# Optimization experiments

Measured on AMD Instinct MI355X. Metric: run time of the kernel, lower is better.

Reference implementation:

```python
import jax, jax.numpy as jnp
import numpy as np

N = 50000        # nodes
E = 800000       # edges (avg degree 16)
F_IN = 128       # num_features
DIM = 128        # hidden dim
C = 10           # num_classes
TEMP = 0.6       # EntropyLinear default temperature
SLOPE = 0.01     # F.leaky_relu default negative slope


def setup_inputs() -> dict:
    key = jax.random.key(0)
    ks = jax.random.split(key, 12)
    x = jax.random.normal(ks[0], (N, F_IN), dtype=jnp.float32)
    edge_index = jax.random.randint(ks[1], (2, E), 0, N, dtype=jnp.int32)
    s_in = 1.0 / np.sqrt(F_IN)
    s_d = 1.0 / np.sqrt(DIM)
    W0 = jax.random.normal(ks[2], (F_IN, DIM), jnp.float32) * s_in
    b0 = jnp.zeros((DIM,), jnp.float32)
    W1 = jax.random.normal(ks[3], (DIM, DIM), jnp.float32) * s_d
    b1 = jnp.zeros((DIM,), jnp.float32)
    W2 = jax.random.normal(ks[4], (DIM, DIM), jnp.float32) * s_d
    b2 = jnp.zeros((DIM,), jnp.float32)
    W3 = jax.random.normal(ks[5], (DIM, DIM), jnp.float32) * s_d
    b3 = jnp.zeros((DIM,), jnp.float32)
    lens_w = jax.random.normal(ks[6], (C, 1, DIM), jnp.float32) * s_d  # (n_classes, out=1, in)
    lens_b = jax.random.normal(ks[7], (C, 1, 1), jnp.float32) * 0.01
    return dict(x=x, edge_index=edge_index, W0=W0, b0=b0, W1=W1, b1=b1,
                W2=W2, b2=b2, W3=W3, b3=b3, lens_w=lens_w, lens_b=lens_b)


def _gcn_conv(h, W, b, src, dst, norm):
    # PyG GCNConv: h' = scatter_add( norm_e * (h W)[src] ) + b
    m = h @ W                                  # [N, out]
    msg = m[src] * norm[:, None]               # [E+N, out] gather + scale
    agg = jax.ops.segment_sum(msg, dst, num_segments=N)
    return agg + b


def reference(x, edge_index, W0, b0, W1, b1, W2, b2, W3, b3, lens_w, lens_b):
    loops = jnp.arange(N, dtype=edge_index.dtype)
    src = jnp.concatenate([edge_index[0], loops])   # add self-loops
    dst = jnp.concatenate([edge_index[1], loops])
    deg = jax.ops.segment_sum(jnp.ones_like(dst, jnp.float32), dst, num_segments=N)
    dis = jnp.where(deg > 0, jax.lax.rsqrt(jnp.maximum(deg, 1.0)), 0.0)
    norm = dis[src] * dis[dst]                      # symmetric D^-1/2 A D^-1/2

    h = x
    for W, b in ((W0, b0), (W1, b1), (W2, b2), (W3, b3)):
        h = _gcn_conv(h, W, b, src, dst, norm)
        h = jax.nn.leaky_relu(h, SLOPE)

    p = jax.nn.softmax(h, axis=-1)
    concepts = p / jnp.max(p, axis=-1, keepdims=True)   # [N, DIM]

    # torch_explain EntropyLinear(DIM, 1, n_classes=C)
    gamma = jnp.abs(lens_w).sum(axis=1)                 # [C, DIM] L1 over out_features
    alpha = jax.nn.softmax(gamma / TEMP, axis=1)
    alpha_norm = alpha / jnp.max(alpha, axis=1, keepdims=True)
    z = concepts[None, :, :] * alpha_norm[:, None, :]   # [C, N, DIM]
    out = jnp.einsum('cnd,cod->cno', z, lens_w) + lens_b  # [C, N, 1]
    out = jnp.transpose(out, (1, 0, 2))                 # [N, C, 1]

    log_probs = jax.nn.log_softmax(out, axis=0).squeeze(-1)  # softmax over nodes
    return concepts, log_probs
```

## Files before the change

kernel.cpp:

```cpp
#include <hip/hip_runtime.h>


#define DIMF 128
#define GRID 1024
#define TPB  256

typedef __bf16 bf16x8 __attribute__((ext_vector_type(8)));
typedef float f32x4 __attribute__((ext_vector_type(4)));

static __device__ __forceinline__ ushort f2bf(float f) {
    uint u = __float_as_uint(f);
    u += 0x7fffu + ((u >> 16) & 1u);
    return (ushort)(u >> 16);
}
static __device__ __forceinline__ float bflo(uint u) { return __uint_as_float(u << 16); }
static __device__ __forceinline__ float bfhi(uint u) { return __uint_as_float(u & 0xffff0000u); }

static __device__ __forceinline__ void upadd(float* acc, const int4& u) {
    const uint* w = (const uint*)&u;
#pragma unroll
    for (int k = 0; k < 4; ++k) {
        acc[2 * k]     += bflo(w[k]);
        acc[2 * k + 1] += bfhi(w[k]);
    }
}


union SMem {
    ushort ws[16384];
    struct { int h[256]; } ha;
    struct { int tmp[256]; } sc;
    struct { int h[256]; int lb[256]; } sa;
    struct { int cnt[256]; int cur[256]; int tmp[256]; } pb;
    struct { float wcT[1280]; float lb[16]; } ep;
    struct { float2 red[4]; } r1;
    struct { float red[2]; } wc;
    struct { float2 red2[176]; float Ls[16]; } l3;
};


static __device__ __forceinline__ void gsync(uint* cb, uint r, uint& pop, uint xcc) {
    __syncthreads();
    if (threadIdx.x == 0) {
        uint* axc   = cb + 128 + 32 * xcc;
        uint* xdone = cb + 640 + 32 * xcc;
        uint* root  = cb + 32;
        if (pop == 0) {
            while (__hip_atomic_load(cb, __ATOMIC_RELAXED, __HIP_MEMORY_SCOPE_AGENT) < (uint)GRID)
                __builtin_amdgcn_s_sleep(2);
            pop = __hip_atomic_load(cb + 64 + xcc, __ATOMIC_RELAXED, __HIP_MEMORY_SCOPE_AGENT);
        }
        uint v = __hip_atomic_fetch_add(axc, 1u, __ATOMIC_RELAXED, __HIP_MEMORY_SCOPE_AGENT) + 1;
        if (v == r * pop) {
            __hip_atomic_fetch_add(root, pop, __ATOMIC_RELEASE, __HIP_MEMORY_SCOPE_AGENT);
            while (__hip_atomic_load(root, __ATOMIC_RELAXED, __HIP_MEMORY_SCOPE_AGENT) < r * (uint)GRID)
                __builtin_amdgcn_s_sleep(2);
            asm volatile("buffer_inv\n\tbuffer_inv sc1\n\ts_waitcnt vmcnt(0)" ::: "memory");
            __hip_atomic_store(xdone, r, __ATOMIC_RELAXED, __HIP_MEMORY_SCOPE_AGENT);
        } else {
            while (__hip_atomic_load(xdone, __ATOMIC_RELAXED, __HIP_MEMORY_SCOPE_AGENT) < r)
                __builtin_amdgcn_s_sleep(2);
            asm volatile("buffer_inv\n\ts_waitcnt vmcnt(0)" ::: "memory");
        }
    }
    __syncthreads();
}


static __device__ __forceinline__ void ldws(ushort* ws, const ushort* WTsL, int tid) {
    const int4* src = (const int4*)WTsL;
    int4* dst = (int4*)ws;
#pragma unroll
    for (int i = 0; i < 8; ++i) dst[tid + 256 * i] = src[tid + 256 * i];
}

static __device__ __forceinline__ void mfma_store(const ushort* ws, const int4* a,
        const float* dis, ushort* M, int nrows, int it, int tid) {
    int wave = tid >> 6, lane = tid & 63;
    int lo = lane & 15, hi = lane >> 4;
    f32x4 acc[8];
#pragma unroll
    for (int ct = 0; ct < 8; ++ct) acc[ct] = (f32x4){0.f, 0.f, 0.f, 0.f};
#pragma unroll
    for (int kc = 0; kc < 4; ++kc) {
        bf16x8 av = __builtin_bit_cast(bf16x8, a[kc]);
#pragma unroll
        for (int ct = 0; ct < 8; ++ct) {
            int col = ct * 16 + lo;
            int byte = (col * 256 + kc * 64 + hi * 16) ^ ((col & 7) << 4);
            bf16x8 bv = *(const bf16x8*)((const char*)ws + byte);
            acc[ct] = __builtin_amdgcn_mfma_f32_16x16x32_bf16(av, bv, acc[ct], 0, 0, 0);
        }
    }
    int rbase = it * 64 + wave * 16 + hi * 4;
#pragma unroll
    for (int r = 0; r < 4; ++r) {
        int orow = rbase + r;
        if (orow < nrows) {
            float dn = dis[orow];
#pragma unroll
            for (int ct = 0; ct < 8; ++ct)
                M[((size_t)(ct >> 1) * nrows + orow) * 32 + (ct & 1) * 16 + lo]
                    = f2bf(dn * acc[ct][r]);
        }
    }
}

static __device__ __forceinline__ void gemm_phase(ushort* ws, const ushort* H,
        const ushort* WTsL, const float* dis, ushort* M, int n, int bid, int tid) {
    int nI = (n + 63) >> 6;
    for (int it = bid; it < nI; it += GRID) {
        __syncthreads();
        ldws(ws, WTsL, tid);
        int wave = tid >> 6, lane = tid & 63;
        int lo = lane & 15, hi = lane >> 4;
        int arow = it * 64 + wave * 16 + lo;
        bool inb = arow < n;
        int4 a[4];
        const int4* h4 = (const int4*)H;
#pragma unroll
        for (int kc = 0; kc < 4; ++kc) {
            int4 z = {0, 0, 0, 0};
            a[kc] = inb ? h4[((size_t)kc * n + arow) * 4 + hi] : z;
        }
        __syncthreads();
        mfma_store(ws, a, dis, M, n, it, tid);
    }
}

static __device__ __forceinline__ void gemm0_phase(ushort* ws, const float* X,
        const ushort* WTsL, const float* dis, ushort* M, int n, int bid, int tid) {
    int nI = (n + 63) >> 6;
    for (int it = bid; it < nI; it += GRID) {
        __syncthreads();
        ldws(ws, WTsL, tid);
        int wave = tid >> 6, lane = tid & 63;
        int lo = lane & 15, hi = lane >> 4;
        int arow = it * 64 + wave * 16 + lo;
        bool inb = arow < n;
        int4 a[4];
        const float4* x4 = (const float4*)X;
#pragma unroll
        for (int kc = 0; kc < 4; ++kc) {
            float4 f0 = make_float4(0.f, 0.f, 0.f, 0.f), f1 = f0;
            if (inb) {
                f0 = x4[(size_t)arow * 32 + kc * 8 + hi * 2];
                f1 = x4[(size_t)arow * 32 + kc * 8 + hi * 2 + 1];
            }
            ushort u[8] = { f2bf(f0.x), f2bf(f0.y), f2bf(f0.z), f2bf(f0.w),
                            f2bf(f1.x), f2bf(f1.y), f2bf(f1.z), f2bf(f1.w) };
            a[kc] = *(const int4*)u;
        }
        __syncthreads();
        mfma_store(ws, a, dis, M, n, it, tid);
    }
}


static __device__ __forceinline__ void agg_phase(const int4* Ms4, const ushort* csr,
        const int* offs, const float* dis, const float* bias, int4* Hs4,
        int n, int bid, int tid) {
    int nI = ((n + 63) >> 6) * 4;
    for (int it = bid; it < nI; it += GRID) {
        int slice = it & 3;
        int node = (it >> 2) * 64 + (tid >> 2);
        if (node >= n) continue;
        int q = tid & 3;
        const int4* M = Ms4 + (size_t)slice * n * 4;
        int beg = offs[node], end = offs[node + 1];

        float acc[8];
        {
            int4 u = M[(size_t)node * 4 + q];
            const uint* w = (const uint*)&u;
#pragma unroll
            for (int k = 0; k < 4; ++k) { acc[2 * k] = bflo(w[k]); acc[2 * k + 1] = bfhi(w[k]); }
        }

        int ee = beg;
        for (; ee + 4 <= end; ee += 4) {
            int s0 = csr[ee], s1 = csr[ee + 1], s2 = csr[ee + 2], s3 = csr[ee + 3];
            int4 u0 = M[(size_t)s0 * 4 + q];
            int4 u1 = M[(size_t)s1 * 4 + q];
            int4 u2 = M[(size_t)s2 * 4 + q];
            int4 u3 = M[(size_t)s3 * 4 + q];
            upadd(acc, u0); upadd(acc, u1); upadd(acc, u2); upadd(acc, u3);
        }
        for (; ee < end; ++ee) {
            int4 u0 = M[(size_t)csr[ee] * 4 + q];
            upadd(acc, u0);
        }

        float dn = dis[node];
        const float2* b2 = (const float2*)bias + slice * 16 + q * 4;
        uint o[4];
#pragma unroll
        for (int k = 0; k < 4; ++k) {
            float2 bk = b2[k];
            float v0 = dn * acc[2 * k] + bk.x, v1 = dn * acc[2 * k + 1] + bk.y;
            v0 = v0 > 0.f ? v0 : 0.01f * v0;
            v1 = v1 > 0.f ? v1 : 0.01f * v1;
            o[k] = (uint)f2bf(v0) | ((uint)f2bf(v1) << 16);
        }
        Hs4[(size_t)slice * n * 4 + (size_t)node * 4 + q] = *(const int4*)o;
    }
}


__global__ __launch_bounds__(TPB, 4) void mega_k(
        const float* __restrict__ x, const int* __restrict__ esrc,
        const int* __restrict__ edst,
        const float* __restrict__ W0f, const float* __restrict__ W1f,
        const float* __restrict__ W2f, const float* __restrict__ W3f,
        const float* __restrict__ b0, const float* __restrict__ b1,
        const float* __restrict__ b2, const float* __restrict__ b3,
        const float* __restrict__ lens_w, const float* __restrict__ lens_b,
        uint* cb, int* bcnt, int* gbase, int* gcur, int* offs, float* dis,
        uint* stage, ushort* csr, ushort* mbuf, ushort* hA, ushort* hB,
        ushort* WTs, float* outbuf, float* wcomb, float2* part,
        float* conc, float* logp, int n, int e, int ncls) {
    __shared__ SMem sm;
    const int bid = blockIdx.x;
    const int tid = threadIdx.x;
    const int NB = (n + 255) >> 8;
    const int EB = (e + 1023) >> 10;
    uint rr = 0;

    uint xcc;
    asm volatile("s_getreg_b32 %0, hwreg(HW_REG_XCC_ID)" : "=s"(xcc));
    xcc &= 15;
    uint pop = 0;
    if (tid == 0) {
        __hip_atomic_fetch_add(cb + 64 + xcc, 1u, __ATOMIC_RELAXED, __HIP_MEMORY_SCOPE_AGENT);
        asm volatile("s_waitcnt vmcnt(0)" ::: "memory");
        __hip_atomic_fetch_add(cb, 1u, __ATOMIC_RELAXED, __HIP_MEMORY_SCOPE_AGENT);
    }

    {
        int nI = EB + 256 + ncls;
        for (int it = bid; it < nI; it += GRID) {
            __syncthreads();
            if (it < EB) {
                sm.ha.h[tid] = 0;
                __syncthreads();
                int base = it * 1024;
#pragma unroll
                for (int k = 0; k < 4; ++k) {
                    int i = base + k * 256 + tid;
                    if (i < e) atomicAdd(&sm.ha.h[edst[i] >> 8], 1);
                }
                __syncthreads();
                if (sm.ha.h[tid]) atomicAdd(&bcnt[tid], sm.ha.h[tid]);
            } else if (it < EB + 256) {
                int wi = it - EB;
                const float* W = (wi >= 192) ? W3f : (wi >= 128) ? W2f
                               : (wi >= 64) ? W1f : W0f;
                ushort* outp = WTs + (size_t)(wi >> 6) * 16384;
                int idx = (wi & 63) * 256 + tid;
                int col = idx >> 7, k = idx & 127;
                float w = W[k * 128 + col];
                int byte = ((col * 128 + k) * 2) ^ ((col & 7) << 4);
                *(ushort*)((char*)outp + byte) = f2bf(w);
            } else {
                int c = it - EB - 256;
                float w = 0.f, g = 0.f, m = -1.f;
                if (tid < 128) { w = lens_w[c * 128 + tid]; g = fabsf(w); m = g; }
#pragma unroll
                for (int off = 32; off; off >>= 1) m = fmaxf(m, __shfl_xor(m, off));
                if (tid < 128 && (tid & 63) == 0) sm.wc.red[tid >> 6] = m;
                __syncthreads();
                if (tid < 128) {
                    m = fmaxf(sm.wc.red[0], sm.wc.red[1]);
                    wcomb[c * 128 + tid] = __expf((g - m) * (1.0f / 0.6f)) * w;
                }
            }
        }
    }
    gsync(cb, ++rr, pop, xcc);

    if (bid == 0) {
        int v = (tid < NB) ? bcnt[tid] : 0;
        sm.sc.tmp[tid] = v;
        __syncthreads();
        int run = v;
        for (int off = 1; off < 256; off <<= 1) {
            int a = (tid >= off) ? sm.sc.tmp[tid - off] : 0;
            __syncthreads();
            run += a;
            sm.sc.tmp[tid] = run;
            __syncthreads();
        }
        if (tid < NB) { gbase[tid] = run - v; gcur[tid] = run - v; }
        if (tid == 0) gbase[NB] = e;
    }
    gsync(cb, ++rr, pop, xcc);

    for (int it = bid; it < EB; it += GRID) {
        __syncthreads();
        sm.sa.h[tid] = 0;
        __syncthreads();
        int base = it * 1024;
        int r[4], bk[4];
        uint val[4];
#pragma unroll
        for (int k = 0; k < 4; ++k) {
            int i = base + k * 256 + tid;
            if (i < e) {
                int s = esrc[i], d = edst[i];
                bk[k] = d >> 8;
                val[k] = ((uint)(d & 255) << 16) | (uint)s;
                r[k] = atomicAdd(&sm.sa.h[bk[k]], 1);
            } else bk[k] = -1;
        }
        __syncthreads();
        if (sm.sa.h[tid]) sm.sa.lb[tid] = atomicAdd(&gcur[tid], sm.sa.h[tid]);
        __syncthreads();
#pragma unroll
        for (int k = 0; k < 4; ++k)
            if (bk[k] >= 0) stage[sm.sa.lb[bk[k]] + r[k]] = val[k];
    }
    gsync(cb, ++rr, pop, xcc);

    for (int it = bid; it < NB; it += GRID) {
        __syncthreads();
        int e0 = gbase[it], e1 = gbase[it + 1];
        sm.pb.cnt[tid] = 0;
        __syncthreads();
        for (int i = e0 + tid; i < e1; i += 256) atomicAdd(&sm.pb.cnt[stage[i] >> 16], 1);
        __syncthreads();
        int v = sm.pb.cnt[tid];
        int run = v;
        sm.pb.tmp[tid] = run;
        __syncthreads();
        for (int off = 1; off < 256; off <<= 1) {
            int a = (tid >= off) ? sm.pb.tmp[tid - off] : 0;
            __syncthreads();
            run += a;
            sm.pb.tmp[tid] = run;
            __syncthreads();
        }
        int ex = e0 + run - v;
        int node = it * 256 + tid;
        if (node < n) {
            offs[node] = ex;
            dis[node] = rsqrtf((float)(v + 1));
        }
        sm.pb.cur[tid] = ex;
        __syncthreads();
        for (int i = e0 + tid; i < e1; i += 256) {
            uint w = stage[i];
            int slot = atomicAdd(&sm.pb.cur[w >> 16], 1);
            csr[slot] = (ushort)(w & 0xffffu);
        }
        if (it == 0 && tid == 0) offs[n] = e;
    }
    gsync(cb, ++rr, pop, xcc);

    gemm0_phase(sm.ws, x, WTs, dis, mbuf, n, bid, tid);
    gsync(cb, ++rr, pop, xcc);
    agg_phase((const int4*)mbuf, csr, offs, dis, b0, (int4*)hA, n, bid, tid);
    gsync(cb, ++rr, pop, xcc);
    gemm_phase(sm.ws, hA, WTs + 16384, dis, mbuf, n, bid, tid);
    gsync(cb, ++rr, pop, xcc);
    agg_phase((const int4*)mbuf, csr, offs, dis, b1, (int4*)hB, n, bid, tid);
    gsync(cb, ++rr, pop, xcc);
    gemm_phase(sm.ws, hB, WTs + 2 * 16384, dis, mbuf, n, bid, tid);
    gsync(cb, ++rr, pop, xcc);
    agg_phase((const int4*)mbuf, csr, offs, dis, b2, (int4*)hA, n, bid, tid);
    gsync(cb, ++rr, pop, xcc);
    gemm_phase(sm.ws, hA, WTs + 3 * 16384, dis, mbuf, n, bid, tid);
    gsync(cb, ++rr, pop, xcc);
    agg_phase((const int4*)mbuf, csr, offs, dis, b3, (int4*)hB, n, bid, tid);
    gsync(cb, ++rr, pop, xcc);

    {
        for (int i = tid; i < ncls * 128; i += TPB) {
            int c = i >> 7, d = i & 127;
            sm.ep.wcT[c * 128 + (d & 7) * 16 + (d >> 3)] = wcomb[i];
        }
        if (tid < ncls) sm.ep.lb[tid] = lens_b[tid];
        __syncthreads();
        const int4* Hs4 = (const int4*)hB;
        int nI = (n + 15) >> 4;
        for (int it = bid; it < nI; it += GRID) {
            int node = it * 16 + (tid >> 4);
            if (node >= n) continue;
            int li = tid & 15;
            int slice = li >> 2, q = li & 3;

            int4 u = Hs4[((size_t)slice * n + node) * 4 + q];
            float v[8];
            {
                const uint* w = (const uint*)&u;
#pragma unroll
                for (int k = 0; k < 4; ++k) { v[2 * k] = bflo(w[k]); v[2 * k + 1] = bfhi(w[k]); }
            }
            float m = v[0];
#pragma unroll
            for (int j = 1; j < 8; ++j) m = fmaxf(m, v[j]);
#pragma unroll
            for (int off = 8; off; off >>= 1) m = fmaxf(m, __shfl_xor(m, off));

            float c8[8];
#pragma unroll
            for (int j = 0; j < 8; ++j) c8[j] = __expf(v[j] - m);

            float4* cc = (float4*)(conc + (size_t)node * 128 + li * 8);
            cc[0] = make_float4(c8[0], c8[1], c8[2], c8[3]);
            cc[1] = make_float4(c8[4], c8[5], c8[6], c8[7]);

            for (int c = 0; c < ncls; ++c) {
                float pv = 0.f;
#pragma unroll
                for (int j = 0; j < 8; ++j) pv += c8[j] * sm.ep.wcT[c * 128 + j * 16 + li];
#pragma unroll
                for (int off = 8; off; off >>= 1) pv += __shfl_xor(pv, off);
                if (li == 0) outbuf[(size_t)c * n + node] = pv + sm.ep.lb[c];
            }
        }
    }
    gsync(cb, ++rr, pop, xcc);

    {
        const int nch = 64;
        const int chunk = (n + nch - 1) / nch;
        int nI = nch * ncls;
        for (int it = bid; it < nI; it += GRID) {
            __syncthreads();
            int cx = it & 63, c = it >> 6;
            const float* col = outbuf + (size_t)c * n;
            int i0 = cx * chunk;
            int i1 = min(n, i0 + chunk);
            float m = -3.0e38f, s = 0.f;
            for (int i = i0 + tid; i < i1; i += TPB) {
                float xv = col[i];
                if (xv > m) { s = s * __expf(m - xv) + 1.f; m = xv; }
                else        { s += __expf(xv - m); }
            }
#pragma unroll
            for (int off = 32; off; off >>= 1) {
                float m2 = __shfl_xor(m, off), s2 = __shfl_xor(s, off);
                float mm = fmaxf(m, m2);
                s = s * __expf(m - mm) + s2 * __expf(m2 - mm);
                m = mm;
            }
            int lane = tid & 63, w = tid >> 6;
            if (lane == 0) sm.r1.red[w] = make_float2(m, s);
            __syncthreads();
            if (tid == 0) {
                m = sm.r1.red[0].x; s = sm.r1.red[0].y;
                for (int k = 1; k < 4; ++k) {
                    float m2 = sm.r1.red[k].x, s2 = sm.r1.red[k].y;
                    float mm = fmaxf(m, m2);
                    s = s * __expf(m - mm) + s2 * __expf(m2 - mm);
                    m = mm;
                }
                part[(size_t)c * nch + cx] = make_float2(m, s);
            }
        }
    }
    gsync(cb, ++rr, pop, xcc);

    {
        int c = tid >> 4, j = tid & 15;
        if (tid < ncls * 16) {
            float m = -3.0e38f, s = 0.f;
#pragma unroll
            for (int k = j * 4; k < j * 4 + 4; ++k) {
                float2 pp = part[(size_t)c * 64 + k];
                float mm = fmaxf(m, pp.x);
                s = s * __expf(m - mm) + pp.y * __expf(pp.x - mm);
                m = mm;
            }
            sm.l3.red2[c * 16 + j] = make_float2(m, s);
        }
        __syncthreads();
        if (tid < ncls) {
            float m = -3.0e38f, s = 0.f;
            for (int k = 0; k < 16; ++k) {
                float2 pp = sm.l3.red2[tid * 16 + k];
                float mm = fmaxf(m, pp.x);
                s = s * __expf(m - mm) + pp.y * __expf(pp.x - mm);
                m = mm;
            }
            sm.l3.Ls[tid] = m + __logf(s);
        }
        __syncthreads();
        int nI = (n + 255) >> 8;
        for (int it = bid; it < nI; it += GRID) {
            int i = it * 256 + tid;
            if (i < n)
                for (int c2 = 0; c2 < ncls; ++c2)
                    logp[(size_t)i * ncls + c2] = outbuf[(size_t)c2 * n + i] - sm.l3.Ls[c2];
        }
    }
}


extern "C" void kernel_launch(void* const* d_in, const int* in_sizes, int n_in,
                              void* d_out, int out_size, void* d_ws, size_t ws_size,
                              hipStream_t stream) {
    const int N = in_sizes[0] / DIMF;
    const int E = in_sizes[1] / 2;
    const int C = in_sizes[10] / DIMF;

    const float* x    = (const float*)d_in[0];
    const int*   ei   = (const int*)d_in[1];
    const int*   esrc = ei;
    const int*   edst = ei + E;
    const float* W0 = (const float*)d_in[2];
    const float* W1 = (const float*)d_in[4];
    const float* W2 = (const float*)d_in[6];
    const float* W3 = (const float*)d_in[8];
    const float* b0 = (const float*)d_in[3];
    const float* b1 = (const float*)d_in[5];
    const float* b2 = (const float*)d_in[7];
    const float* b3 = (const float*)d_in[9];
    const float* lens_w = (const float*)d_in[10];
    const float* lens_b = (const float*)d_in[11];

    float* out_concepts = (float*)d_out;
    float* out_logp     = (float*)d_out + (size_t)N * DIMF;

    char* p = (char*)d_ws;
    auto alloc = [&](size_t bytes) -> void* {
        void* r = (void*)p;
        p += (bytes + 255) & ~(size_t)255;
        return r;
    };
    uint*   cb     = (uint*)alloc(8192);
    int*    bcnt   = (int*)alloc(256 * 4);
    int*    gbase  = (int*)alloc(257 * 4);
    int*    gcur   = (int*)alloc(256 * 4);
    int*    offs   = (int*)alloc(((size_t)N + 1) * 4);
    float*  dis    = (float*)alloc((size_t)N * 4);
    uint*   stage  = (uint*)alloc((size_t)E * 4);
    ushort* csr    = (ushort*)alloc((size_t)E * 2);
    ushort* mbuf   = (ushort*)alloc((size_t)N * DIMF * 2);
    ushort* hA     = (ushort*)alloc((size_t)N * DIMF * 2);
    ushort* hB     = (ushort*)alloc((size_t)N * DIMF * 2);
    ushort* WTs    = (ushort*)alloc((size_t)4 * 16384 * 2);
    float*  outbuf = (float*)alloc((size_t)C * N * 4);
    float*  wcomb  = (float*)alloc((size_t)C * DIMF * 4);
    float2* part   = (float2*)alloc((size_t)C * 64 * 8);

    hipMemsetAsync(cb, 0, 8192 + 1024, stream);

    mega_k<<<GRID, TPB, 0, stream>>>(
        x, esrc, edst, W0, W1, W2, W3, b0, b1, b2, b3, lens_w, lens_b,
        cb, bcnt, gbase, gcur, offs, dis, stage, csr, mbuf, hA, hB,
        WTs, outbuf, wcomb, part, out_concepts, out_logp, N, E, C);
}
```

Measured before the change: 285.2 us.

## Fuse aggregation with next-layer GEMM and switch to row-major message layout

Each layer's neighbour aggregation, bias and leaky-ReLU now run in the same block pass as the following layer's MFMA GEMM. The intermediate H buffer round-trip and three grid-wide barriers go away. The message buffer layout changes from four column slices to row-major 256-byte rows, and weights are staged into LDS in quarters so the LDS footprint shrinks to 8 KB. In exchange each lane gathers whole rows with more registers live, and the aggregation now uses a 64-node-per-block mapping that may load-balance worse than the earlier sliced one.

```diff
diff --git a/kernel.cpp b/kernel.cpp
--- a/kernel.cpp
+++ b/kernel.cpp
@@ -27,7 +27,7 @@
 
 
 union SMem {
-    ushort ws[16384];
+    ushort ws[4096];
     struct { int h[256]; } ha;
     struct { int tmp[256]; } sc;
     struct { int h[256]; int lb[256]; } sa;
@@ -67,73 +67,141 @@
 }
 
 
-static __device__ __forceinline__ void ldws(ushort* ws, const ushort* WTsL, int tid) {
-    const int4* src = (const int4*)WTsL;
-    int4* dst = (int4*)ws;
-#pragma unroll
-    for (int i = 0; i < 8; ++i) dst[tid + 256 * i] = src[tid + 256 * i];
-}
-
-static __device__ __forceinline__ void mfma_store(const ushort* ws, const int4* a,
-        const float* dis, ushort* M, int nrows, int it, int tid) {
-    int wave = tid >> 6, lane = tid & 63;
-    int lo = lane & 15, hi = lane >> 4;
-    f32x4 acc[8];
-#pragma unroll
-    for (int ct = 0; ct < 8; ++ct) acc[ct] = (f32x4){0.f, 0.f, 0.f, 0.f};
-#pragma unroll
-    for (int kc = 0; kc < 4; ++kc) {
-        bf16x8 av = __builtin_bit_cast(bf16x8, a[kc]);
-#pragma unroll
-        for (int ct = 0; ct < 8; ++ct) {
-            int col = ct * 16 + lo;
-            int byte = (col * 256 + kc * 64 + hi * 16) ^ ((col & 7) << 4);
-            bf16x8 bv = *(const bf16x8*)((const char*)ws + byte);
-            acc[ct] = __builtin_amdgcn_mfma_f32_16x16x32_bf16(av, bv, acc[ct], 0, 0, 0);
-        }
-    }
+static __device__ __forceinline__ void gemm_quarters(ushort* ws, const ushort* WTsL,
+        const int4* a, f32x4* oacc, int lo, int hi, int tid) {
+#pragma unroll
+    for (int q = 0; q < 4; ++q) {
+        __syncthreads();
+        {
+            const int4* src = (const int4*)(WTsL + q * 4096);
+            int4* dst = (int4*)ws;
+            dst[tid] = src[tid];
+            dst[tid + 256] = src[tid + 256];
+        }
+        __syncthreads();
+#pragma unroll
+        for (int kc = 0; kc < 4; ++kc) {
+            bf16x8 av = __builtin_bit_cast(bf16x8, a[kc]);
+#pragma unroll
+            for (int ctl = 0; ctl < 2; ++ctl) {
+                int coll = ctl * 16 + lo;
+                int byte = (coll * 256 + kc * 64 + hi * 16) ^ ((coll & 7) << 4);
+                bf16x8 bv = *(const bf16x8*)((const char*)ws + byte);
+                oacc[q * 2 + ctl] =
+                    __builtin_amdgcn_mfma_f32_16x16x32_bf16(av, bv, oacc[q * 2 + ctl], 0, 0, 0);
+            }
+        }
+    }
+}
+
+static __device__ __forceinline__ void store_m(const f32x4* oacc, const float* dis,
+        ushort* M, int n, int it, int wave, int lo, int hi) {
     int rbase = it * 64 + wave * 16 + hi * 4;
 #pragma unroll
     for (int r = 0; r < 4; ++r) {
         int orow = rbase + r;
-        if (orow < nrows) {
+        if (orow < n) {
             float dn = dis[orow];
 #pragma unroll
-            for (int ct = 0; ct < 8; ++ct)
-                M[((size_t)(ct >> 1) * nrows + orow) * 32 + (ct & 1) * 16 + lo]
-                    = f2bf(dn * acc[ct][r]);
-        }
-    }
-}
-
-static __device__ __forceinline__ void gemm_phase(ushort* ws, const ushort* H,
-        const ushort* WTsL, const float* dis, ushort* M, int n, int bid, int tid) {
+            for (int g = 0; g < 8; ++g)
+                M[(size_t)orow * 128 + g * 16 + lo] = f2bf(dn * oacc[g][r]);
+        }
+    }
+}
+
+
+static __device__ __forceinline__ void fused_phase(ushort* ws, const ushort* Mcur,
+        const ushort* WTsL, const ushort* __restrict__ csr, const int* __restrict__ offs,
+        const float* __restrict__ dis, const float* __restrict__ bias,
+        ushort* Mnext, bool do_gemm, int n, int bid, int tid) {
     int nI = (n + 63) >> 6;
     for (int it = bid; it < nI; it += GRID) {
-        __syncthreads();
-        ldws(ws, WTsL, tid);
         int wave = tid >> 6, lane = tid & 63;
         int lo = lane & 15, hi = lane >> 4;
-        int arow = it * 64 + wave * 16 + lo;
-        bool inb = arow < n;
+        int node = it * 64 + wave * 16 + lo;
+        bool inb = node < n;
+        float acc[4][8];
+        const char* Mb = (const char*)Mcur;
+
+        if (inb) {
+#pragma unroll
+            for (int kc = 0; kc < 4; ++kc) {
+                int4 u = *(const int4*)(Mb + (size_t)node * 256 + kc * 64 + hi * 16);
+                const uint* w = (const uint*)&u;
+#pragma unroll
+                for (int k2 = 0; k2 < 4; ++k2) {
+                    acc[kc][2 * k2] = bflo(w[k2]);
+                    acc[kc][2 * k2 + 1] = bfhi(w[k2]);
+                }
+            }
+            int beg = offs[node], end = offs[node + 1];
+            int ee = beg;
+            for (; ee + 2 <= end; ee += 2) {
+                int s0 = csr[ee], s1 = csr[ee + 1];
+                int4 u[8];
+#pragma unroll
+                for (int kc = 0; kc < 4; ++kc) {
+                    u[kc]     = *(const int4*)(Mb + (size_t)s0 * 256 + kc * 64 + hi * 16);
+                    u[4 + kc] = *(const int4*)(Mb + (size_t)s1 * 256 + kc * 64 + hi * 16);
+                }
+#pragma unroll
+                for (int kc = 0; kc < 4; ++kc) { upadd(acc[kc], u[kc]); upadd(acc[kc], u[4 + kc]); }
+            }
+            for (; ee < end; ++ee) {
+                int s0 = csr[ee];
+#pragma unroll
+                for (int kc = 0; kc < 4; ++kc) {
+                    int4 u = *(const int4*)(Mb + (size_t)s0 * 256 + kc * 64 + hi * 16);
+                    upadd(acc[kc], u);
+                }
+            }
+            float dn = dis[node];
+#pragma unroll
+            for (int kc = 0; kc < 4; ++kc)
+#pragma unroll
+                for (int j = 0; j < 8; ++j) {
+                    float v = dn * acc[kc][j] + bias[kc * 32 + hi * 8 + j];
+                    acc[kc][j] = v > 0.f ? v : 0.01f * v;
+                }
+        } else {
+#pragma unroll
+            for (int kc = 0; kc < 4; ++kc)
+#pragma unroll
+                for (int j = 0; j < 8; ++j) acc[kc][j] = 0.f;
+        }
+
         int4 a[4];
-        const int4* h4 = (const int4*)H;
 #pragma unroll
         for (int kc = 0; kc < 4; ++kc) {
-            int4 z = {0, 0, 0, 0};
-            a[kc] = inb ? h4[((size_t)kc * n + arow) * 4 + hi] : z;
-        }
-        __syncthreads();
-        mfma_store(ws, a, dis, M, n, it, tid);
-    }
-}
-
-static __device__ __forceinline__ void gemm0_phase(ushort* ws, const float* X,
-        const ushort* WTsL, const float* dis, ushort* M, int n, int bid, int tid) {
+            ushort u8[8] = { f2bf(acc[kc][0]), f2bf(acc[kc][1]), f2bf(acc[kc][2]),
+                             f2bf(acc[kc][3]), f2bf(acc[kc][4]), f2bf(acc[kc][5]),
+                             f2bf(acc[kc][6]), f2bf(acc[kc][7]) };
+            a[kc] = *(const int4*)u8;
+        }
+
+        if (!do_gemm) {
+            if (inb) {
+#pragma unroll
+                for (int kc = 0; kc < 4; ++kc)
+                    *(int4*)((char*)Mnext + (size_t)node * 256 + kc * 64 + hi * 16) = a[kc];
+            }
+            continue;
+        }
+
+        f32x4 oacc[8];
+#pragma unroll
+        for (int g = 0; g < 8; ++g) oacc[g] = (f32x4){0.f, 0.f, 0.f, 0.f};
+        gemm_quarters(ws, WTsL, a, oacc, lo, hi, tid);
+        store_m(oacc, dis, Mnext, n, it, wave, lo, hi);
+    }
+}
+
+
+static __device__ __forceinline__ void gemm0_phase(ushort* ws, const float* __restrict__ X,
+        const ushort* WTsL, const float* __restrict__ dis, ushort* M,
+        int n, int bid, int tid) {
     int nI = (n + 63) >> 6;
     for (int it = bid; it < nI; it += GRID) {
-        __syncthreads();
-        ldws(ws, WTsL, tid);
         int wave = tid >> 6, lane = tid & 63;
         int lo = lane & 15, hi = lane >> 4;
         int arow = it * 64 + wave * 16 + lo;
@@ -151,58 +219,11 @@
                             f2bf(f1.x), f2bf(f1.y), f2bf(f1.z), f2bf(f1.w) };
             a[kc] = *(const int4*)u;
         }
-        __syncthreads();
-        mfma_store(ws, a, dis, M, n, it, tid);
-    }
-}
-
-
-static __device__ __forceinline__ void agg_phase(const int4* Ms4, const ushort* csr,
-        const int* offs, const float* dis, const float* bias, int4* Hs4,
-        int n, int bid, int tid) {
-    int nI = ((n + 63) >> 6) * 4;
-    for (int it = bid; it < nI; it += GRID) {
-        int slice = it & 3;
-        int node = (it >> 2) * 64 + (tid >> 2);
-        if (node >= n) continue;
-        int q = tid & 3;
-        const int4* M = Ms4 + (size_t)slice * n * 4;
-        int beg = offs[node], end = offs[node + 1];
-
-        float acc[8];
-        {
-            int4 u = M[(size_t)node * 4 + q];
-            const uint* w = (const uint*)&u;
-#pragma unroll
-            for (int k = 0; k < 4; ++k) { acc[2 * k] = bflo(w[k]); acc[2 * k + 1] = bfhi(w[k]); }
-        }
-
-        int ee = beg;
-        for (; ee + 4 <= end; ee += 4) {
-            int s0 = csr[ee], s1 = csr[ee + 1], s2 = csr[ee + 2], s3 = csr[ee + 3];
-            int4 u0 = M[(size_t)s0 * 4 + q];
-            int4 u1 = M[(size_t)s1 * 4 + q];
-            int4 u2 = M[(size_t)s2 * 4 + q];
-            int4 u3 = M[(size_t)s3 * 4 + q];
-            upadd(acc, u0); upadd(acc, u1); upadd(acc, u2); upadd(acc, u3);
-        }
-        for (; ee < end; ++ee) {
-            int4 u0 = M[(size_t)csr[ee] * 4 + q];
-            upadd(acc, u0);
-        }
-
-        float dn = dis[node];
-        const float2* b2 = (const float2*)bias + slice * 16 + q * 4;
-        uint o[4];
-#pragma unroll
-        for (int k = 0; k < 4; ++k) {
-            float2 bk = b2[k];
-            float v0 = dn * acc[2 * k] + bk.x, v1 = dn * acc[2 * k + 1] + bk.y;
-            v0 = v0 > 0.f ? v0 : 0.01f * v0;
-            v1 = v1 > 0.f ? v1 : 0.01f * v1;
-            o[k] = (uint)f2bf(v0) | ((uint)f2bf(v1) << 16);
-        }
-        Hs4[(size_t)slice * n * 4 + (size_t)node * 4 + q] = *(const int4*)o;
+        f32x4 oacc[8];
+#pragma unroll
+        for (int g = 0; g < 8; ++g) oacc[g] = (f32x4){0.f, 0.f, 0.f, 0.f};
+        gemm_quarters(ws, WTsL, a, oacc, lo, hi, tid);
+        store_m(oacc, dis, M, n, it, wave, lo, hi);
     }
 }
 
@@ -216,7 +237,7 @@
         const float* __restrict__ b2, const float* __restrict__ b3,
         const float* __restrict__ lens_w, const float* __restrict__ lens_b,
         uint* cb, int* bcnt, int* gbase, int* gcur, int* offs, float* dis,
-        uint* stage, ushort* csr, ushort* mbuf, ushort* hA, ushort* hB,
+        uint* stage, ushort* csr, ushort* mbufA, ushort* mbufB,
         ushort* WTs, float* outbuf, float* wcomb, float2* part,
         float* conc, float* logp, int n, int e, int ncls) {
     __shared__ SMem sm;
@@ -356,21 +377,15 @@
     }
     gsync(cb, ++rr, pop, xcc);
 
-    gemm0_phase(sm.ws, x, WTs, dis, mbuf, n, bid, tid);
-    gsync(cb, ++rr, pop, xcc);
-    agg_phase((const int4*)mbuf, csr, offs, dis, b0, (int4*)hA, n, bid, tid);
-    gsync(cb, ++rr, pop, xcc);
-    gemm_phase(sm.ws, hA, WTs + 16384, dis, mbuf, n, bid, tid);
-    gsync(cb, ++rr, pop, xcc);
-    agg_phase((const int4*)mbuf, csr, offs, dis, b1, (int4*)hB, n, bid, tid);
-    gsync(cb, ++rr, pop, xcc);
-    gemm_phase(sm.ws, hB, WTs + 2 * 16384, dis, mbuf, n, bid, tid);
-    gsync(cb, ++rr, pop, xcc);
-    agg_phase((const int4*)mbuf, csr, offs, dis, b2, (int4*)hA, n, bid, tid);
-    gsync(cb, ++rr, pop, xcc);
-    gemm_phase(sm.ws, hA, WTs + 3 * 16384, dis, mbuf, n, bid, tid);
-    gsync(cb, ++rr, pop, xcc);
-    agg_phase((const int4*)mbuf, csr, offs, dis, b3, (int4*)hB, n, bid, tid);
+    gemm0_phase(sm.ws, x, WTs, dis, mbufA, n, bid, tid);
+    gsync(cb, ++rr, pop, xcc);
+    fused_phase(sm.ws, mbufA, WTs + 16384, csr, offs, dis, b0, mbufB, true, n, bid, tid);
+    gsync(cb, ++rr, pop, xcc);
+    fused_phase(sm.ws, mbufB, WTs + 2 * 16384, csr, offs, dis, b1, mbufA, true, n, bid, tid);
+    gsync(cb, ++rr, pop, xcc);
+    fused_phase(sm.ws, mbufA, WTs + 3 * 16384, csr, offs, dis, b2, mbufB, true, n, bid, tid);
+    gsync(cb, ++rr, pop, xcc);
+    fused_phase(sm.ws, mbufB, nullptr, csr, offs, dis, b3, mbufA, false, n, bid, tid);
     gsync(cb, ++rr, pop, xcc);
 
     {
@@ -380,15 +395,14 @@
         }
         if (tid < ncls) sm.ep.lb[tid] = lens_b[tid];
         __syncthreads();
-        const int4* Hs4 = (const int4*)hB;
+        const int4* Hs4 = (const int4*)mbufA;
         int nI = (n + 15) >> 4;
         for (int it = bid; it < nI; it += GRID) {
             int node = it * 16 + (tid >> 4);
             if (node >= n) continue;
             int li = tid & 15;
-            int slice = li >> 2, q = li & 3;
-
-            int4 u = Hs4[((size_t)slice * n + node) * 4 + q];
+
+            int4 u = Hs4[(size_t)node * 16 + li];
             float v[8];
             {
                 const uint* w = (const uint*)&u;
@@ -536,9 +550,8 @@
     float*  dis    = (float*)alloc((size_t)N * 4);
     uint*   stage  = (uint*)alloc((size_t)E * 4);
     ushort* csr    = (ushort*)alloc((size_t)E * 2);
-    ushort* mbuf   = (ushort*)alloc((size_t)N * DIMF * 2);
-    ushort* hA     = (ushort*)alloc((size_t)N * DIMF * 2);
-    ushort* hB     = (ushort*)alloc((size_t)N * DIMF * 2);
+    ushort* mbufA  = (ushort*)alloc((size_t)N * DIMF * 2);
+    ushort* mbufB  = (ushort*)alloc((size_t)N * DIMF * 2);
     ushort* WTs    = (ushort*)alloc((size_t)4 * 16384 * 2);
     float*  outbuf = (float*)alloc((size_t)C * N * 4);
     float*  wcomb  = (float*)alloc((size_t)C * DIMF * 4);
@@ -548,6 +561,6 @@
 
     mega_k<<<GRID, TPB, 0, stream>>>(
         x, esrc, edst, W0, W1, W2, W3, b0, b1, b2, b3, lens_w, lens_b,
-        cb, bcnt, gbase, gcur, offs, dis, stage, csr, mbuf, hA, hB,
+        cb, bcnt, gbase, gcur, offs, dis, stage, csr, mbufA, mbufB,
         WTs, outbuf, wcomb, part, out_concepts, out_logp, N, E, C);
 }
```

Result: slower. 297.3 us (+4.2%).

## Shrink weight LDS tile to quarters and size persistent grid from occupancy

Applied to the files above, without the earlier changes.

The GEMM phases now stage the 128x128 bf16 weight matrix in shared memory in four 8 KB quarters instead of one 32 KB tile, computing two column tiles per quarter. This cuts the shared-memory union so more blocks can be resident per CU. The grid size is then taken from the occupancy API (capped at 8 blocks per CU times 256 CUs) rather than a fixed 1024, and the grid barrier uses gridDim. The cost is extra __syncthreads and weight reloads per quarter inside every GEMM tile, plus a heavier grid barrier as more blocks take part in it.

```diff
diff --git a/kernel.cpp b/kernel.cpp
--- a/kernel.cpp
+++ b/kernel.cpp
@@ -2,7 +2,6 @@
 
 
 #define DIMF 128
-#define GRID 1024
 #define TPB  256
 
 typedef __bf16 bf16x8 __attribute__((ext_vector_type(8)));
@@ -27,7 +26,7 @@
 
 
 union SMem {
-    ushort ws[16384];
+    ushort ws[4096];
     struct { int h[256]; } ha;
     struct { int tmp[256]; } sc;
     struct { int h[256]; int lb[256]; } sa;
@@ -39,21 +38,21 @@
 };
 
 
-static __device__ __forceinline__ void gsync(uint* cb, uint r, uint& pop, uint xcc) {
+static __device__ __forceinline__ void gsync(uint* cb, uint r, uint& pop, uint xcc, uint gsz) {
     __syncthreads();
     if (threadIdx.x == 0) {
         uint* axc   = cb + 128 + 32 * xcc;
         uint* xdone = cb + 640 + 32 * xcc;
         uint* root  = cb + 32;
         if (pop == 0) {
-            while (__hip_atomic_load(cb, __ATOMIC_RELAXED, __HIP_MEMORY_SCOPE_AGENT) < (uint)GRID)
+            while (__hip_atomic_load(cb, __ATOMIC_RELAXED, __HIP_MEMORY_SCOPE_AGENT) < gsz)
                 __builtin_amdgcn_s_sleep(2);
             pop = __hip_atomic_load(cb + 64 + xcc, __ATOMIC_RELAXED, __HIP_MEMORY_SCOPE_AGENT);
         }
         uint v = __hip_atomic_fetch_add(axc, 1u, __ATOMIC_RELAXED, __HIP_MEMORY_SCOPE_AGENT) + 1;
         if (v == r * pop) {
             __hip_atomic_fetch_add(root, pop, __ATOMIC_RELEASE, __HIP_MEMORY_SCOPE_AGENT);
-            while (__hip_atomic_load(root, __ATOMIC_RELAXED, __HIP_MEMORY_SCOPE_AGENT) < r * (uint)GRID)
+            while (__hip_atomic_load(root, __ATOMIC_RELAXED, __HIP_MEMORY_SCOPE_AGENT) < r * gsz)
                 __builtin_amdgcn_s_sleep(2);
             asm volatile("buffer_inv\n\tbuffer_inv sc1\n\ts_waitcnt vmcnt(0)" ::: "memory");
             __hip_atomic_store(xdone, r, __ATOMIC_RELAXED, __HIP_MEMORY_SCOPE_AGENT);
@@ -67,51 +66,53 @@
 }
 
 
-static __device__ __forceinline__ void ldws(ushort* ws, const ushort* WTsL, int tid) {
-    const int4* src = (const int4*)WTsL;
-    int4* dst = (int4*)ws;
-#pragma unroll
-    for (int i = 0; i < 8; ++i) dst[tid + 256 * i] = src[tid + 256 * i];
-}
-
-static __device__ __forceinline__ void mfma_store(const ushort* ws, const int4* a,
-        const float* dis, ushort* M, int nrows, int it, int tid) {
-    int wave = tid >> 6, lane = tid & 63;
-    int lo = lane & 15, hi = lane >> 4;
-    f32x4 acc[8];
-#pragma unroll
-    for (int ct = 0; ct < 8; ++ct) acc[ct] = (f32x4){0.f, 0.f, 0.f, 0.f};
-#pragma unroll
-    for (int kc = 0; kc < 4; ++kc) {
-        bf16x8 av = __builtin_bit_cast(bf16x8, a[kc]);
-#pragma unroll
-        for (int ct = 0; ct < 8; ++ct) {
-            int col = ct * 16 + lo;
-            int byte = (col * 256 + kc * 64 + hi * 16) ^ ((col & 7) << 4);
-            bf16x8 bv = *(const bf16x8*)((const char*)ws + byte);
-            acc[ct] = __builtin_amdgcn_mfma_f32_16x16x32_bf16(av, bv, acc[ct], 0, 0, 0);
-        }
-    }
+static __device__ __forceinline__ void gemm_quarters(ushort* ws, const ushort* WTsL,
+        const int4* a, f32x4* oacc, int lo, int hi, int tid) {
+#pragma unroll
+    for (int q = 0; q < 4; ++q) {
+        __syncthreads();
+        {
+            const int4* src = (const int4*)(WTsL + q * 4096);
+            int4* dst = (int4*)ws;
+            dst[tid] = src[tid];
+            dst[tid + 256] = src[tid + 256];
+        }
+        __syncthreads();
+#pragma unroll
+        for (int kc = 0; kc < 4; ++kc) {
+            bf16x8 av = __builtin_bit_cast(bf16x8, a[kc]);
+#pragma unroll
+            for (int ctl = 0; ctl < 2; ++ctl) {
+                int coll = ctl * 16 + lo;
+                int byte = (coll * 256 + kc * 64 + hi * 16) ^ ((coll & 7) << 4);
+                bf16x8 bv = *(const bf16x8*)((const char*)ws + byte);
+                oacc[q * 2 + ctl] =
+                    __builtin_amdgcn_mfma_f32_16x16x32_bf16(av, bv, oacc[q * 2 + ctl], 0, 0, 0);
+            }
+        }
+    }
+}
+
+static __device__ __forceinline__ void store_m_sliced(const f32x4* oacc, const float* dis,
+        ushort* M, int n, int it, int wave, int lo, int hi) {
     int rbase = it * 64 + wave * 16 + hi * 4;
 #pragma unroll
     for (int r = 0; r < 4; ++r) {
         int orow = rbase + r;
-        if (orow < nrows) {
+        if (orow < n) {
             float dn = dis[orow];
 #pragma unroll
-            for (int ct = 0; ct < 8; ++ct)
-                M[((size_t)(ct >> 1) * nrows + orow) * 32 + (ct & 1) * 16 + lo]
-                    = f2bf(dn * acc[ct][r]);
+            for (int g = 0; g < 8; ++g)
+                M[((size_t)(g >> 1) * n + orow) * 32 + (g & 1) * 16 + lo]
+                    = f2bf(dn * oacc[g][r]);
         }
     }
 }
 
 static __device__ __forceinline__ void gemm_phase(ushort* ws, const ushort* H,
-        const ushort* WTsL, const float* dis, ushort* M, int n, int bid, int tid) {
+        const ushort* WTsL, const float* dis, ushort* M, int n, int bid, int tid, int gsz) {
     int nI = (n + 63) >> 6;
-    for (int it = bid; it < nI; it += GRID) {
-        __syncthreads();
-        ldws(ws, WTsL, tid);
+    for (int it = bid; it < nI; it += gsz) {
         int wave = tid >> 6, lane = tid & 63;
         int lo = lane & 15, hi = lane >> 4;
         int arow = it * 64 + wave * 16 + lo;
@@ -123,17 +124,18 @@
             int4 z = {0, 0, 0, 0};
             a[kc] = inb ? h4[((size_t)kc * n + arow) * 4 + hi] : z;
         }
-        __syncthreads();
-        mfma_store(ws, a, dis, M, n, it, tid);
-    }
-}
-
-static __device__ __forceinline__ void gemm0_phase(ushort* ws, const float* X,
-        const ushort* WTsL, const float* dis, ushort* M, int n, int bid, int tid) {
+        f32x4 oacc[8];
+#pragma unroll
+        for (int g = 0; g < 8; ++g) oacc[g] = (f32x4){0.f, 0.f, 0.f, 0.f};
+        gemm_quarters(ws, WTsL, a, oacc, lo, hi, tid);
+        store_m_sliced(oacc, dis, M, n, it, wave, lo, hi);
+    }
+}
+
+static __device__ __forceinline__ void gemm0_phase(ushort* ws, const float* __restrict__ X,
+        const ushort* WTsL, const float* dis, ushort* M, int n, int bid, int tid, int gsz) {
     int nI = (n + 63) >> 6;
-    for (int it = bid; it < nI; it += GRID) {
-        __syncthreads();
-        ldws(ws, WTsL, tid);
+    for (int it = bid; it < nI; it += gsz) {
         int wave = tid >> 6, lane = tid & 63;
         int lo = lane & 15, hi = lane >> 4;
         int arow = it * 64 + wave * 16 + lo;
@@ -151,17 +153,20 @@
                             f2bf(f1.x), f2bf(f1.y), f2bf(f1.z), f2bf(f1.w) };
             a[kc] = *(const int4*)u;
         }
-        __syncthreads();
-        mfma_store(ws, a, dis, M, n, it, tid);
+        f32x4 oacc[8];
+#pragma unroll
+        for (int g = 0; g < 8; ++g) oacc[g] = (f32x4){0.f, 0.f, 0.f, 0.f};
+        gemm_quarters(ws, WTsL, a, oacc, lo, hi, tid);
+        store_m_sliced(oacc, dis, M, n, it, wave, lo, hi);
     }
 }
 
 
 static __device__ __forceinline__ void agg_phase(const int4* Ms4, const ushort* csr,
         const int* offs, const float* dis, const float* bias, int4* Hs4,
-        int n, int bid, int tid) {
+        int n, int bid, int tid, int gsz) {
     int nI = ((n + 63) >> 6) * 4;
-    for (int it = bid; it < nI; it += GRID) {
+    for (int it = bid; it < nI; it += gsz) {
         int slice = it & 3;
         int node = (it >> 2) * 64 + (tid >> 2);
         if (node >= n) continue;
@@ -222,6 +227,7 @@
     __shared__ SMem sm;
     const int bid = blockIdx.x;
     const int tid = threadIdx.x;
+    const int gsz = gridDim.x;
     const int NB = (n + 255) >> 8;
     const int EB = (e + 1023) >> 10;
     uint rr = 0;
@@ -238,7 +244,7 @@
 
     {
         int nI = EB + 256 + ncls;
-        for (int it = bid; it < nI; it += GRID) {
+        for (int it = bid; it < nI; it += gsz) {
             __syncthreads();
             if (it < EB) {
                 sm.ha.h[tid] = 0;
@@ -276,7 +282,7 @@
             }
         }
     }
-    gsync(cb, ++rr, pop, xcc);
+    gsync(cb, ++rr, pop, xcc, gsz);
 
     if (bid == 0) {
         int v = (tid < NB) ? bcnt[tid] : 0;
@@ -293,9 +299,9 @@
         if (tid < NB) { gbase[tid] = run - v; gcur[tid] = run - v; }
         if (tid == 0) gbase[NB] = e;
     }
-    gsync(cb, ++rr, pop, xcc);
-
-    for (int it = bid; it < EB; it += GRID) {
+    gsync(cb, ++rr, pop, xcc, gsz);
+
+    for (int it = bid; it < EB; it += gsz) {
         __syncthreads();
         sm.sa.h[tid] = 0;
         __syncthreads();
@@ -319,9 +325,9 @@
         for (int k = 0; k < 4; ++k)
             if (bk[k] >= 0) stage[sm.sa.lb[bk[k]] + r[k]] = val[k];
     }
-    gsync(cb, ++rr, pop, xcc);
-
-    for (int it = bid; it < NB; it += GRID) {
+    gsync(cb, ++rr, pop, xcc, gsz);
+
+    for (int it = bid; it < NB; it += gsz) {
         __syncthreads();
         int e0 = gbase[it], e1 = gbase[it + 1];
         sm.pb.cnt[tid] = 0;
@@ -354,24 +360,24 @@
         }
         if (it == 0 && tid == 0) offs[n] = e;
     }
-    gsync(cb, ++rr, pop, xcc);
-
-    gemm0_phase(sm.ws, x, WTs, dis, mbuf, n, bid, tid);
-    gsync(cb, ++rr, pop, xcc);
-    agg_phase((const int4*)mbuf, csr, offs, dis, b0, (int4*)hA, n, bid, tid);
-    gsync(cb, ++rr, pop, xcc);
-    gemm_phase(sm.ws, hA, WTs + 16384, dis, mbuf, n, bid, tid);
-    gsync(cb, ++rr, pop, xcc);
-    agg_phase((const int4*)mbuf, csr, offs, dis, b1, (int4*)hB, n, bid, tid);
-    gsync(cb, ++rr, pop, xcc);
-    gemm_phase(sm.ws, hB, WTs + 2 * 16384, dis, mbuf, n, bid, tid);
-    gsync(cb, ++rr, pop, xcc);
-    agg_phase((const int4*)mbuf, csr, offs, dis, b2, (int4*)hA, n, bid, tid);
-    gsync(cb, ++rr, pop, xcc);
-    gemm_phase(sm.ws, hA, WTs + 3 * 16384, dis, mbuf, n, bid, tid);
-    gsync(cb, ++rr, pop, xcc);
-    agg_phase((const int4*)mbuf, csr, offs, dis, b3, (int4*)hB, n, bid, tid);
-    gsync(cb, ++rr, pop, xcc);
+    gsync(cb, ++rr, pop, xcc, gsz);
+
+    gemm0_phase(sm.ws, x, WTs, dis, mbuf, n, bid, tid, gsz);
+    gsync(cb, ++rr, pop, xcc, gsz);
+    agg_phase((const int4*)mbuf, csr, offs, dis, b0, (int4*)hA, n, bid, tid, gsz);
+    gsync(cb, ++rr, pop, xcc, gsz);
+    gemm_phase(sm.ws, hA, WTs + 16384, dis, mbuf, n, bid, tid, gsz);
+    gsync(cb, ++rr, pop, xcc, gsz);
+    agg_phase((const int4*)mbuf, csr, offs, dis, b1, (int4*)hB, n, bid, tid, gsz);
+    gsync(cb, ++rr, pop, xcc, gsz);
+    gemm_phase(sm.ws, hB, WTs + 2 * 16384, dis, mbuf, n, bid, tid, gsz);
+    gsync(cb, ++rr, pop, xcc, gsz);
+    agg_phase((const int4*)mbuf, csr, offs, dis, b2, (int4*)hA, n, bid, tid, gsz);
+    gsync(cb, ++rr, pop, xcc, gsz);
+    gemm_phase(sm.ws, hA, WTs + 3 * 16384, dis, mbuf, n, bid, tid, gsz);
+    gsync(cb, ++rr, pop, xcc, gsz);
+    agg_phase((const int4*)mbuf, csr, offs, dis, b3, (int4*)hB, n, bid, tid, gsz);
+    gsync(cb, ++rr, pop, xcc, gsz);
 
     {
         for (int i = tid; i < ncls * 128; i += TPB) {
@@ -382,7 +388,7 @@
         __syncthreads();
         const int4* Hs4 = (const int4*)hB;
         int nI = (n + 15) >> 4;
-        for (int it = bid; it < nI; it += GRID) {
+        for (int it = bid; it < nI; it += gsz) {
             int node = it * 16 + (tid >> 4);
             if (node >= n) continue;
             int li = tid & 15;
@@ -419,13 +425,13 @@
             }
         }
     }
-    gsync(cb, ++rr, pop, xcc);
+    gsync(cb, ++rr, pop, xcc, gsz);
 
     {
         const int nch = 64;
         const int chunk = (n + nch - 1) / nch;
         int nI = nch * ncls;
-        for (int it = bid; it < nI; it += GRID) {
+        for (int it = bid; it < nI; it += gsz) {
             __syncthreads();
             int cx = it & 63, c = it >> 6;
             const float* col = outbuf + (size_t)c * n;
@@ -459,7 +465,7 @@
             }
         }
     }
-    gsync(cb, ++rr, pop, xcc);
+    gsync(cb, ++rr, pop, xcc, gsz);
 
     {
         int c = tid >> 4, j = tid & 15;
@@ -487,7 +493,7 @@
         }
         __syncthreads();
         int nI = (n + 255) >> 8;
-        for (int it = bid; it < nI; it += GRID) {
+        for (int it = bid; it < nI; it += gsz) {
             int i = it * 256 + tid;
             if (i < n)
                 for (int c2 = 0; c2 < ncls; ++c2)
@@ -544,9 +550,19 @@
     float*  wcomb  = (float*)alloc((size_t)C * DIMF * 4);
     float2* part   = (float2*)alloc((size_t)C * 64 * 8);
 
+    static int nb_cached = 0;
+    if (nb_cached == 0) {
+        int nb = 0;
+        if (hipOccupancyMaxActiveBlocksPerMultiprocessor(&nb, mega_k, TPB, 0) != hipSuccess || nb < 1)
+            nb = 4;
+        if (nb > 8) nb = 8;
+        nb_cached = nb;
+    }
+    const int GRIDn = nb_cached * 256;
+
     hipMemsetAsync(cb, 0, 8192 + 1024, stream);
 
-    mega_k<<<GRID, TPB, 0, stream>>>(
+    mega_k<<<GRIDn, TPB, 0, stream>>>(
         x, esrc, edst, W0, W1, W2, W3, b0, b1, b2, b3, lens_w, lens_b,
         cb, bcnt, gbase, gcur, offs, dis, stage, csr, mbuf, hA, hB,
         WTs, outbuf, wcomb, part, out_concepts, out_logp, N, E, C);
```

Result: slower. 322.2 us (+13.0%).
